# Kernel optimization log

Hardware: AMD Instinct MI355X
Metric: run time of the kernel (lower is better)

Reference implementation:

```python
import jax, jax.numpy as jnp
import numpy as np

N, D, H, F, T = 2048, 256, 4, 64, 64
HF = H * F


def setup_inputs() -> dict:
    key = jax.random.key(0)
    ks = jax.random.split(key, 24)
    f32 = jnp.float32
    emb = jax.random.normal(ks[0], (N, D), f32)
    y_as_x = jax.random.normal(ks[1], (N, T), f32)
    adj = (jax.random.uniform(ks[2], (N, N)) < 0.02).astype(f32)
    u = lambda k, shape, s: jax.random.uniform(k, shape, f32, -s, s)
    stdv = 1.0 / np.sqrt(HF)
    inp = dict(emb=emb, y_as_x=y_as_x, adj=adj)
    for i, p in enumerate(['pos', 'neg']):
        o = 3 + i * 6
        inp[p + '_w'] = u(ks[o], (D, HF), stdv)
        inp[p + '_wu'] = u(ks[o + 1], (H, F), 1.0)
        inp[p + '_wv'] = u(ks[o + 2], (H, F), 1.0)
        inp[p + '_b'] = u(ks[o + 3], (1, HF), stdv)
        inp[p + '_pw'] = u(ks[o + 4], (D, HF), 0.02)
        inp[p + '_pb'] = jnp.zeros((HF,), f32)
    inp['self_w'] = u(ks[15], (D, D), 0.02)
    inp['self_b'] = jnp.zeros((D,), f32)
    inp['mlp_pos_w'] = u(ks[16], (HF, D), 0.02)
    inp['mlp_pos_b'] = jnp.zeros((D,), f32)
    inp['mlp_neg_w'] = u(ks[17], (HF, D), 0.02)
    inp['mlp_neg_b'] = jnp.zeros((D,), f32)
    inp['sem_w1'] = u(ks[18], (D, D), 0.02)
    inp['sem_b1'] = jnp.zeros((D,), f32)
    inp['sem_w2'] = u(ks[19], (D, 1), 0.02)
    return inp


def _gat(x, mask, w, wu, wv, b, pw, pb):
    # x: [N,D], mask: [N,N] bool; multi-head GAT with dense masked softmax
    s = (x @ w).reshape(N, H, F).transpose(1, 0, 2)          # [H,N,F]
    f1 = jnp.einsum('hnf,hf->hn', s, wu)                     # u-score per node
    f2 = jnp.einsum('hnf,hf->hn', s, wv)                     # v-score per node
    logits = f1[:, None, :] + f2[:, :, None]                 # [H,N,N], i<-j
    logits = jax.nn.leaky_relu(logits, 0.2)
    masked = jnp.where(mask[None], logits, -1e9)
    attn = jnp.where(mask[None], jax.nn.softmax(masked, axis=2), 0.0)
    out = jnp.einsum('hij,hjf->hif', attn, s)                # [H,N,F]
    out = out.transpose(1, 0, 2).reshape(N, HF) + b
    return out + x @ pw + pb


def reference(emb, y_as_x, adj, pos_w, pos_wu, pos_wv, pos_b, pos_pw, pos_pb,
              neg_w, neg_wu, neg_wv, neg_b, neg_pw, neg_pb,
              self_w, self_b, mlp_pos_w, mlp_pos_b, mlp_neg_w, mlp_neg_b,
              sem_w1, sem_b1, sem_w2):
    # batched pairwise correlation (replaces the per-node Python loop)
    yc = y_as_x - y_as_x.mean(axis=1, keepdims=True)         # centered
    dot = yc @ yc.T                                          # [N,N]
    std = jnp.sqrt((yc ** 2).sum(axis=1) / (T - 1))          # torch std: ddof=1
    corr = dot / (std[:, None] * std[None, :])
    edge = adj != 0
    pos_mask = edge & (corr >= 0.1)
    neg_mask = edge & (corr < 0.1)

    pos_sup = _gat(emb, pos_mask, pos_w, pos_wu, pos_wv, pos_b, pos_pw, pos_pb)
    neg_sup = _gat(emb, neg_mask, neg_w, neg_wu, neg_wv, neg_b, neg_pw, neg_pb)

    sup = emb @ self_w + self_b
    pos_sup = pos_sup @ mlp_pos_w + mlp_pos_b
    neg_sup = neg_sup @ mlp_neg_w + mlp_neg_b

    all_emb = jnp.stack((sup, pos_sup, neg_sup), axis=1)     # [N,3,D]
    # semantic attention over the 3 relation channels
    wlog = jnp.tanh(all_emb @ sem_w1 + sem_b1) @ sem_w2      # [N,3,1]
    beta = jax.nn.softmax(wlog, axis=1)
    x = (beta * all_emb).sum(axis=1)                         # [N,D]
    # PairNorm PN-SI
    x = x - x.mean(axis=0)
    rownorm = jnp.sqrt(1e-6 + (x ** 2).sum(axis=1, keepdims=True))
    return x / rownorm
```

## Files before the change

### kernel.cpp

```cpp
#include <hip/hip_runtime.h>
#include <hip/hip_bf16.h>

#define KN  2048
#define KD  256
#define KH  4
#define KF  64
#define KT  64
#define NCS 32
#define MAXE 256

typedef __attribute__((ext_vector_type(8))) short short8;
typedef __attribute__((ext_vector_type(4))) float floatx4;

struct Args {
    const float *y, *adj, *emb;
    const float *pos_w, *pos_wu, *pos_wv, *pos_b, *pos_pw, *pos_pb;
    const float *neg_w, *neg_wu, *neg_wv, *neg_b, *neg_pw, *neg_pb;
    const float *self_w, *self_b;
    const float *mlp_pos_w, *mlp_pos_b, *mlp_neg_w, *mlp_neg_b;
    const float *sem_w1, *sem_b1, *sem_w2;
    float* out;
    unsigned char* code;
    float *ycs, *S_pos, *S_neg, *P_pos, *P_neg, *sup, *G, *psup, *X, *colsum;
    float *f1p, *f2p, *f1n, *f2n, *M0Wp, *M0Wn, *fbp, *fbn, *wlog;
};

__device__ __forceinline__ float wave_sum(float v) {
    #pragma unroll
    for (int o = 32; o > 0; o >>= 1) v += __shfl_xor(v, o, 64);
    return v;
}
__device__ __forceinline__ float wave_max(float v) {
    #pragma unroll
    for (int o = 32; o > 0; o >>= 1) v = fmaxf(v, __shfl_xor(v, o, 64));
    return v;
}
__device__ __forceinline__ short f2bs(float x) {
    union { __hip_bfloat16 h; short s; } u;
    u.h = __float2bfloat16(x);
    return u.s;
}

__global__ __launch_bounds__(256) void setup_kernel(const float* __restrict__ y,
                                                    float* __restrict__ ycs) {
    int w = threadIdx.x >> 6, lane = threadIdx.x & 63;
    int n = blockIdx.x * 4 + w;
    float v = y[n * KT + lane];
    float mean = wave_sum(v) * (1.0f / KT);
    float yc = v - mean;
    float ss = wave_sum(yc * yc);
    ycs[n * KT + lane] = yc * rsqrtf(ss * (1.0f / (KT - 1)));
}

__device__ __forceinline__ void corr_body(const float* __restrict__ ycs,
                                          const float* __restrict__ adj,
                                          unsigned char* __restrict__ code,
                                          int blk, char* smem) {
    float (*As)[68] = (float(*)[68])smem;
    float (*Bs)[68] = (float(*)[68])(smem + 4352);
    int bi = 0, rem = blk;
    while (rem >= 32 - bi) { rem -= 32 - bi; bi++; }
    int bj = bi + rem;
    int i0 = bi * 64, j0 = bj * 64;
    int t = threadIdx.x;
    int tx = t & 15, ty = t >> 4;
    int ar = t >> 2, ac = (t & 3) * 4;
    float acc[4][4] = {};
    for (int kt = 0; kt < KT; kt += 16) {
        float4 a4 = *reinterpret_cast<const float4*>(&ycs[(size_t)(i0 + ar) * KT + kt + ac]);
        float4 b4 = *reinterpret_cast<const float4*>(&ycs[(size_t)(j0 + ar) * KT + kt + ac]);
        As[ac + 0][ar] = a4.x; As[ac + 1][ar] = a4.y; As[ac + 2][ar] = a4.z; As[ac + 3][ar] = a4.w;
        Bs[ac + 0][ar] = b4.x; Bs[ac + 1][ar] = b4.y; Bs[ac + 2][ar] = b4.z; Bs[ac + 3][ar] = b4.w;
        __syncthreads();
        #pragma unroll
        for (int kk = 0; kk < 16; kk++) {
            float4 av = *reinterpret_cast<const float4*>(&As[kk][ty * 4]);
            float4 bv = *reinterpret_cast<const float4*>(&Bs[kk][tx * 4]);
            float a4v[4] = {av.x, av.y, av.z, av.w};
            float b4v[4] = {bv.x, bv.y, bv.z, bv.w};
            #pragma unroll
            for (int ii = 0; ii < 4; ii++)
                #pragma unroll
                for (int jj = 0; jj < 4; jj++) acc[ii][jj] += a4v[ii] * b4v[jj];
        }
        __syncthreads();
    }
    #pragma unroll
    for (int ii = 0; ii < 4; ii++) {
        int i = i0 + ty * 4 + ii;
        int jb = j0 + tx * 4;
        float4 av4 = *reinterpret_cast<const float4*>(&adj[(size_t)i * KN + jb]);
        float a4v[4] = {av4.x, av4.y, av4.z, av4.w};
        uchar4 cc;
        unsigned char* c = (unsigned char*)&cc;
        #pragma unroll
        for (int jj = 0; jj < 4; jj++)
            c[jj] = (a4v[jj] != 0.0f) ? ((acc[ii][jj] >= 0.1f) ? 1 : 2) : 0;
        *reinterpret_cast<uchar4*>(&code[(size_t)i * KN + jb]) = cc;
    }
    if (bi != bj) {
        #pragma unroll
        for (int jj = 0; jj < 4; jj++) {
            int j = j0 + tx * 4 + jj;
            int ib = i0 + ty * 4;
            float4 av4 = *reinterpret_cast<const float4*>(&adj[(size_t)j * KN + ib]);
            float a4v[4] = {av4.x, av4.y, av4.z, av4.w};
            uchar4 cc;
            unsigned char* c = (unsigned char*)&cc;
            #pragma unroll
            for (int ii = 0; ii < 4; ii++)
                c[ii] = (a4v[ii] != 0.0f) ? ((acc[ii][jj] >= 0.1f) ? 1 : 2) : 0;
            *reinterpret_cast<uchar4*>(&code[(size_t)j * KN + ib]) = cc;
        }
    }
}

template <bool TANH, int WCH>
__device__ __forceinline__ void mfma_gemm_body(
    const float* __restrict__ A, int lda, int bm,
    const float* __restrict__ B, int ldb, int bn,
    const float* __restrict__ bias,
    float* __restrict__ C, int ldc, int cn,
    float* __restrict__ f1h, float* __restrict__ f2h,
    const float* __restrict__ wu_h, const float* __restrict__ wv_h,
    float* __restrict__ wlogp, const float* __restrict__ w2,
    char* smem)
{
    short* As = (short*)smem;
    short* Bs = (short*)(smem + 5120);
    int t = threadIdx.x;
    int w = t >> 6, lane = t & 63;
    int m16 = lane & 15, kq = lane >> 4;
    floatx4 acc0 = {0,0,0,0}, acc1 = {0,0,0,0}, acc2 = {0,0,0,0}, acc3 = {0,0,0,0};
    int ar = t >> 2, acq = (t & 3) * 8;
    int bnn = t & 63, bkg = (t >> 6) * 8;
    for (int kt = 0; kt < KD; kt += 32) {
        const float* pa = &A[(size_t)(bm + ar) * lda + kt + acq];
        float4 a0 = *(const float4*)pa;
        float4 a1 = *(const float4*)(pa + 4);
        short8 av;
        av[0] = f2bs(a0.x); av[1] = f2bs(a0.y); av[2] = f2bs(a0.z); av[3] = f2bs(a0.w);
        av[4] = f2bs(a1.x); av[5] = f2bs(a1.y); av[6] = f2bs(a1.z); av[7] = f2bs(a1.w);
        const float* pb = &B[(size_t)(kt + bkg) * ldb + bn + bnn];
        short8 bv;
        #pragma unroll
        for (int u = 0; u < 8; u++) bv[u] = f2bs(pb[(size_t)u * ldb]);
        __syncthreads();
        *(short8*)&As[ar * 40 + acq] = av;
        *(short8*)&Bs[bnn * 40 + bkg] = bv;
        __syncthreads();
        short8 af  = *(short8*)&As[(w * 16 + m16) * 40 + kq * 8];
        short8 bf0 = *(short8*)&Bs[( 0 + m16) * 40 + kq * 8];
        short8 bf1 = *(short8*)&Bs[(16 + m16) * 40 + kq * 8];
        short8 bf2 = *(short8*)&Bs[(32 + m16) * 40 + kq * 8];
        short8 bf3 = *(short8*)&Bs[(48 + m16) * 40 + kq * 8];
        acc0 = __builtin_amdgcn_mfma_f32_16x16x32_bf16(af, bf0, acc0, 0, 0, 0);
        acc1 = __builtin_amdgcn_mfma_f32_16x16x32_bf16(af, bf1, acc1, 0, 0, 0);
        acc2 = __builtin_amdgcn_mfma_f32_16x16x32_bf16(af, bf2, acc2, 0, 0, 0);
        acc3 = __builtin_amdgcn_mfma_f32_16x16x32_bf16(af, bf3, acc3, 0, 0, 0);
    }
    int row0 = bm + w * 16 + kq * 4;
    floatx4 accs[4] = {acc0, acc1, acc2, acc3};
    if (WCH >= 0) {
        float w2c[4];
        #pragma unroll
        for (int nb = 0; nb < 4; nb++) w2c[nb] = w2[cn + nb * 16 + m16];
        #pragma unroll
        for (int r = 0; r < 4; r++) {
            float p = 0.0f;
            #pragma unroll
            for (int nb = 0; nb < 4; nb++) {
                float v = accs[nb][r] + bias[nb * 16 + m16];
                float vc = fminf(fmaxf(v, -9.0f), 9.0f);
                float ex = __expf(2.0f * vc);
                p += ((ex - 1.0f) / (ex + 1.0f)) * w2c[nb];
            }
            #pragma unroll
            for (int o = 1; o < 16; o <<= 1) p += __shfl_xor(p, o, 64);
            if (m16 == 0) atomicAdd(&wlogp[(size_t)(row0 + r) * 4 + WCH], p);
        }
        return;
    }
    #pragma unroll
    for (int nb = 0; nb < 4; nb++) {
        #pragma unroll
        for (int r = 0; r < 4; r++) {
            int col = nb * 16 + m16;
            float v = accs[nb][r] + (bias ? bias[col] : 0.0f);
            if (TANH) {
                float vc = fminf(fmaxf(v, -9.0f), 9.0f);
                float ex = __expf(2.0f * vc);
                v = (ex - 1.0f) / (ex + 1.0f);
            }
            C[(size_t)(row0 + r) * ldc + cn + col] = v;
        }
    }
    if (f1h) {
        float wuv[4], wvv[4];
        #pragma unroll
        for (int nb = 0; nb < 4; nb++) { wuv[nb] = wu_h[nb * 16 + m16]; wvv[nb] = wv_h[nb * 16 + m16]; }
        #pragma unroll
        for (int r = 0; r < 4; r++) {
            float p1 = accs[0][r] * wuv[0] + accs[1][r] * wuv[1] + accs[2][r] * wuv[2] + accs[3][r] * wuv[3];
            float p2 = accs[0][r] * wvv[0] + accs[1][r] * wvv[1] + accs[2][r] * wvv[2] + accs[3][r] * wvv[3];
            #pragma unroll
            for (int o = 1; o < 16; o <<= 1) {
                p1 += __shfl_xor(p1, o, 64);
                p2 += __shfl_xor(p2, o, 64);
            }
            if (m16 == 0) { f1h[row0 + r] = p1; f2h[row0 + r] = p2; }
        }
    }
}

__device__ __forceinline__ void fb_unit(const float* __restrict__ mb,
                                        const float* __restrict__ w1,
                                        const float* __restrict__ b1,
                                        float* __restrict__ fb) {
    int j = threadIdx.x;
    float acc = b1[j];
    for (int k = 0; k < KD; k++) acc = fmaf(mb[k], w1[(size_t)k * KD + j], acc);
    fb[j] = acc;
}

__global__ __launch_bounds__(256, 4) void phase1_kernel(Args a) {
    __shared__ alignas(16) char smem[10240];
    int blk = blockIdx.x;
    if (blk < 528) { corr_body(a.ycs, a.adj, a.code, blk, smem); return; }
    if (blk < 1168) {
        int b = blk - 528;
        int tn = b % 20, tm = b / 20;
        int buf = tn >> 2, coloff = (tn & 3) * 64, h = tn & 3;
        const float* B; const float* bias = nullptr; float* C;
        float *f1h = nullptr, *f2h = nullptr;
        const float *wu = nullptr, *wv = nullptr;
        if (buf == 0) {
            B = a.pos_w; C = a.S_pos;
            f1h = a.f1p + h * KN; f2h = a.f2p + h * KN;
            wu = a.pos_wu + h * KF; wv = a.pos_wv + h * KF;
        } else if (buf == 1) {
            B = a.neg_w; C = a.S_neg;
            f1h = a.f1n + h * KN; f2h = a.f2n + h * KN;
            wu = a.neg_wu + h * KF; wv = a.neg_wv + h * KF;
        } else if (buf == 2) { B = a.pos_pw; bias = a.pos_pb + coloff; C = a.P_pos; }
        else if (buf == 3)   { B = a.neg_pw; bias = a.neg_pb + coloff; C = a.P_neg; }
        else                 { B = a.self_w; bias = a.self_b + coloff; C = a.sup; }
        mfma_gemm_body<false, -1>(a.emb, KD, tm * 64, B, KD, coloff, bias,
                                  C, KD, coloff, f1h, f2h, wu, wv,
                                  nullptr, nullptr, smem);
        return;
    }
    if (blk < 1184) {
        int v = blk - 1168;
        mfma_gemm_body<false, -1>(a.mlp_pos_w, KD, (v >> 2) * 64, a.sem_w1, KD, (v & 3) * 64,
                                  nullptr, a.M0Wp, KD, (v & 3) * 64,
                                  nullptr, nullptr, nullptr, nullptr,
                                  nullptr, nullptr, smem);
        return;
    }
    if (blk < 1200) {
        int v = blk - 1184;
        mfma_gemm_body<false, -1>(a.mlp_neg_w, KD, (v >> 2) * 64, a.sem_w1, KD, (v & 3) * 64,
                                  nullptr, a.M0Wn, KD, (v & 3) * 64,
                                  nullptr, nullptr, nullptr, nullptr,
                                  nullptr, nullptr, smem);
        return;
    }
    if (blk == 1200) { fb_unit(a.mlp_pos_b, a.sem_w1, a.sem_b1, a.fbp); return; }
    if (blk == 1201) { fb_unit(a.mlp_neg_b, a.sem_w1, a.sem_b1, a.fbn); return; }
    for (int j = threadIdx.x; j < NCS * KD; j += 256) a.colsum[j] = 0.0f;
    for (int j = threadIdx.x; j < KN * 4; j += 256) a.wlog[j] = 0.0f;
}

__global__ __launch_bounds__(256) void attn_kernel(Args a) {
    __shared__ alignas(16) int jl[2][MAXE];
    __shared__ alignas(16) float lg[KH][MAXE];
    __shared__ int cnt[2];
    int i = blockIdx.x;
    int w = threadIdx.x >> 6, lane = threadIdx.x & 63;
    if (threadIdx.x < 2) cnt[threadIdx.x] = 0;
    __syncthreads();
    #pragma unroll
    for (int it = 0; it < 2; it++) {
        int base = w * 512 + it * 256;
        uchar4 cv = *reinterpret_cast<const uchar4*>(&a.code[(size_t)i * KN + base + lane * 4]);
        const unsigned char* ce = (const unsigned char*)&cv;
        #pragma unroll
        for (int e = 0; e < 4; e++) {
            #pragma unroll
            for (int rel = 0; rel < 2; rel++) {
                bool pr = (ce[e] == (rel ? (unsigned char)2 : (unsigned char)1));
                unsigned long long bal = __ballot(pr);
                int tot = __popcll(bal);
                int basepos = 0;
                if (lane == 0 && tot) basepos = atomicAdd(&cnt[rel], tot);
                basepos = __shfl(basepos, 0, 64);
                if (pr) {
                    int idx = basepos + __popcll(bal & ((1ull << lane) - 1ull));
                    if (idx < MAXE) jl[rel][idx] = base + lane * 4 + e;
                }
            }
        }
    }
    __syncthreads();
    int c0 = cnt[0]; if (c0 > MAXE) c0 = MAXE;
    int c1 = cnt[1]; if (c1 > MAXE) c1 = MAXE;
    if (threadIdx.x < 4) {
        int cR = (c0 + 3) & ~3;
        if (c0 + threadIdx.x < cR) jl[0][c0 + threadIdx.x] = 0;
    } else if (threadIdx.x < 8) {
        int l2 = threadIdx.x - 4;
        int cR = (c1 + 3) & ~3;
        if (c1 + l2 < cR) jl[1][c1 + l2] = 0;
    }
    __syncthreads();
    int h = w;
    int g = lane >> 4, q4 = (lane & 15) * 4;
    for (int rel = 0; rel < 2; rel++) {
        const float* f1 = rel ? a.f1n : a.f1p;
        const float* f2 = rel ? a.f2n : a.f2p;
        const float* S  = rel ? a.S_neg : a.S_pos;
        const float* P  = rel ? a.P_neg : a.P_pos;
        const float* b  = rel ? a.neg_b : a.pos_b;
        float* G        = a.G + (size_t)rel * KN * KD;
        int count = rel ? c1 : c0;
        int countR = (count + 3) & ~3;
        float f2i = f2[h * KN + i];
        float m = -1e30f;
        for (int k = lane; k < count; k += 64) {
            int j = jl[rel][k];
            float x = f1[h * KN + j] + f2i;
            x = (x > 0.0f) ? x : 0.2f * x;
            lg[h][k] = x;
            m = fmaxf(m, x);
        }
        m = wave_max(m);
        float ps = 0.0f;
        for (int k = lane; k < count; k += 64) {
            float e = __expf(lg[h][k] - m);
            lg[h][k] = e;
            ps += e;
        }
        float denom = wave_sum(ps);
        for (int k2 = count + lane; k2 < countR; k2 += 64) lg[h][k2] = 0.0f;
        const float* Sh4 = S + h * KF + q4;
        float ax = 0.0f, ay = 0.0f, az = 0.0f, aw = 0.0f;
        for (int k = 0; k < countR; k += 4) {
            int j = jl[rel][k + g];
            float wgt = lg[h][k + g];
            float4 sv = *reinterpret_cast<const float4*>(&Sh4[(size_t)j * KD]);
            ax += wgt * sv.x; ay += wgt * sv.y; az += wgt * sv.z; aw += wgt * sv.w;
        }
        #pragma unroll
        for (int o = 16; o < 64; o <<= 1) {
            ax += __shfl_xor(ax, o, 64); ay += __shfl_xor(ay, o, 64);
            az += __shfl_xor(az, o, 64); aw += __shfl_xor(aw, o, 64);
        }
        if (g == 0) {
            float inv = count ? (1.0f / denom) : 0.0f;
            int col = h * KF + q4;
            size_t idx = (size_t)i * KD + col;
            float4 pv = *reinterpret_cast<const float4*>(&P[idx]);
            float4 o4;
            o4.x = ax * inv + b[col + 0] + pv.x;
            o4.y = ay * inv + b[col + 1] + pv.y;
            o4.z = az * inv + b[col + 2] + pv.z;
            o4.w = aw * inv + b[col + 3] + pv.w;
            *reinterpret_cast<float4*>(&G[idx]) = o4;
        }
    }
}

__global__ __launch_bounds__(256, 4) void tail_kernel(Args a) {
    __shared__ alignas(16) char smem[10240];
    int u = blockIdx.x;
    if (u < 256) {
        int bx = u & 3, bm = (u >> 2) * 64;
        bool sel = bm >= KN;
        mfma_gemm_body<false, -1>(a.G, KD, bm, sel ? a.mlp_neg_w : a.mlp_pos_w, KD, bx * 64,
                                  (sel ? a.mlp_neg_b : a.mlp_pos_b) + bx * 64,
                                  a.psup, KD, bx * 64,
                                  nullptr, nullptr, nullptr, nullptr,
                                  nullptr, nullptr, smem);
    } else if (u < 384) {
        int v = u - 256; int bx = v & 3, bm = (v >> 2) * 64;
        mfma_gemm_body<true, 0>(a.sup, KD, bm, a.sem_w1, KD, bx * 64, a.sem_b1 + bx * 64,
                                nullptr, KD, bx * 64,
                                nullptr, nullptr, nullptr, nullptr,
                                a.wlog, a.sem_w2, smem);
    } else if (u < 512) {
        int v = u - 384; int bx = v & 3, bm = (v >> 2) * 64;
        mfma_gemm_body<true, 1>(a.G, KD, bm, a.M0Wp, KD, bx * 64, a.fbp + bx * 64,
                                nullptr, KD, bx * 64,
                                nullptr, nullptr, nullptr, nullptr,
                                a.wlog, a.sem_w2, smem);
    } else {
        int v = u - 512; int bx = v & 3, bm = KN + (v >> 2) * 64;
        mfma_gemm_body<true, 2>(a.G, KD, bm, a.M0Wn, KD, bx * 64, a.fbn + bx * 64,
                                nullptr, KD, bx * 64,
                                nullptr, nullptr, nullptr, nullptr,
                                a.wlog - (size_t)KN * 4, a.sem_w2, smem);
    }
}

__global__ __launch_bounds__(256) void combine_kernel(Args a) {
    int n = blockIdx.x, d = threadIdx.x;
    size_t idx = (size_t)n * KD + d;
    float4 wl = *reinterpret_cast<const float4*>(&a.wlog[(size_t)n * 4]);
    float mm = fmaxf(wl.x, fmaxf(wl.y, wl.z));
    float e0 = __expf(wl.x - mm), e1 = __expf(wl.y - mm), e2 = __expf(wl.z - mm);
    float inv = 1.0f / (e0 + e1 + e2);
    float* nsup = a.psup + (size_t)KN * KD;
    float x = (e0 * inv) * a.sup[idx] + (e1 * inv) * a.psup[idx] + (e2 * inv) * nsup[idx];
    a.X[idx] = x;
    atomicAdd(&a.colsum[(n & (NCS - 1)) * KD + d], x);
}

__global__ __launch_bounds__(256) void final_kernel(Args a) {
    __shared__ float sb[4];
    int n = blockIdx.x, d = threadIdx.x;
    float cs = 0.0f;
    #pragma unroll
    for (int r = 0; r < NCS; r++) cs += a.colsum[r * KD + d];
    float mean = cs * (1.0f / KN);
    float xc = a.X[(size_t)n * KD + d] - mean;
    int wv = d >> 6, lane = d & 63;
    float s = wave_sum(xc * xc);
    if (lane == 0) sb[wv] = s;
    __syncthreads();
    float ss = sb[0] + sb[1] + sb[2] + sb[3];
    a.out[(size_t)n * KD + d] = xc * rsqrtf(1e-6f + ss);
}

extern "C" void kernel_launch(void* const* d_in, const int* in_sizes, int n_in,
                              void* d_out, int out_size, void* d_ws, size_t ws_size,
                              hipStream_t stream) {
    typedef const float* fp;
    Args a;
    a.emb    = (fp)d_in[0];
    a.y      = (fp)d_in[1];
    a.adj    = (fp)d_in[2];
    a.pos_w  = (fp)d_in[3];  a.pos_wu = (fp)d_in[4];  a.pos_wv = (fp)d_in[5];
    a.pos_b  = (fp)d_in[6];  a.pos_pw = (fp)d_in[7];  a.pos_pb = (fp)d_in[8];
    a.neg_w  = (fp)d_in[9];  a.neg_wu = (fp)d_in[10]; a.neg_wv = (fp)d_in[11];
    a.neg_b  = (fp)d_in[12]; a.neg_pw = (fp)d_in[13]; a.neg_pb = (fp)d_in[14];
    a.self_w = (fp)d_in[15]; a.self_b = (fp)d_in[16];
    a.mlp_pos_w = (fp)d_in[17]; a.mlp_pos_b = (fp)d_in[18];
    a.mlp_neg_w = (fp)d_in[19]; a.mlp_neg_b = (fp)d_in[20];
    a.sem_w1 = (fp)d_in[21]; a.sem_b1 = (fp)d_in[22]; a.sem_w2 = (fp)d_in[23];
    a.out = (float*)d_out;

    char* ws = (char*)d_ws;
    size_t off = 0;
    auto alloc = [&](size_t sz) -> char* {
        char* p = ws + off;
        off += (sz + 511) & ~(size_t)511;
        return p;
    };
    const size_t MAT = (size_t)KN * KD * 4;

    a.ycs    = (float*)alloc((size_t)KN * KT * 4);
    a.code   = (unsigned char*)alloc((size_t)KN * KN);
    a.S_pos  = (float*)alloc(MAT);
    a.S_neg  = (float*)alloc(MAT);
    a.P_pos  = (float*)alloc(MAT);
    a.P_neg  = (float*)alloc(MAT);
    a.sup    = (float*)alloc(MAT);
    a.G      = (float*)alloc(2 * MAT);
    a.psup   = (float*)alloc(2 * MAT);
    a.X      = (float*)alloc(MAT);
    a.colsum = (float*)alloc((size_t)NCS * KD * 4);
    a.f1p    = (float*)alloc((size_t)KH * KN * 4);
    a.f2p    = (float*)alloc((size_t)KH * KN * 4);
    a.f1n    = (float*)alloc((size_t)KH * KN * 4);
    a.f2n    = (float*)alloc((size_t)KH * KN * 4);
    a.M0Wp   = (float*)alloc((size_t)KD * KD * 4);
    a.M0Wn   = (float*)alloc((size_t)KD * KD * 4);
    a.fbp    = (float*)alloc(KD * 4);
    a.fbn    = (float*)alloc(KD * 4);
    a.wlog   = (float*)alloc((size_t)KN * 4 * 4);

    setup_kernel<<<512, 256, 0, stream>>>(a.y, a.ycs);
    phase1_kernel<<<1203, 256, 0, stream>>>(a);
    attn_kernel<<<KN, 256, 0, stream>>>(a);
    tail_kernel<<<640, 256, 0, stream>>>(a);
    combine_kernel<<<KN, 256, 0, stream>>>(a);
    final_kernel<<<KN, 256, 0, stream>>>(a);
}
```

Before: 163.3 us.

## Fuse correlation normalization into corr tiles and merge combine/final via grid barrier

Drops the separate setup kernel: each correlation tile now computes the row means and inverse stds of its 64+64 y rows and normalizes on the fly while staging into shared memory. The combine and PairNorm kernels are merged into one 1024-block kernel where each block handles two rows, keeps x in registers, and waits on a global atomic counter barrier before reading column sums. This removes two launches and the X intermediate round trip. In exchange, row statistics are recomputed redundantly per tile, and correctness relies on all 1024 blocks being co-resident for the spin barrier.

```diff
diff --git a/kernel.cpp b/kernel.cpp
--- a/kernel.cpp
+++ b/kernel.cpp
@@ -8,6 +8,7 @@
 #define KT  64
 #define NCS 32
 #define MAXE 256
+#define CFB 1024
 
 typedef __attribute__((ext_vector_type(8))) short short8;
 typedef __attribute__((ext_vector_type(4))) float floatx4;
@@ -20,8 +21,9 @@
     const float *mlp_pos_w, *mlp_pos_b, *mlp_neg_w, *mlp_neg_b;
     const float *sem_w1, *sem_b1, *sem_w2;
     float* out;
+    int* bar;
     unsigned char* code;
-    float *ycs, *S_pos, *S_neg, *P_pos, *P_neg, *sup, *G, *psup, *X, *colsum;
+    float *S_pos, *S_neg, *P_pos, *P_neg, *sup, *G, *psup, *colsum;
     float *f1p, *f2p, *f1n, *f2n, *M0Wp, *M0Wn, *fbp, *fbn, *wlog;
 };
 
@@ -41,36 +43,47 @@
     return u.s;
 }
 
-__global__ __launch_bounds__(256) void setup_kernel(const float* __restrict__ y,
-                                                    float* __restrict__ ycs) {
-    int w = threadIdx.x >> 6, lane = threadIdx.x & 63;
-    int n = blockIdx.x * 4 + w;
-    float v = y[n * KT + lane];
-    float mean = wave_sum(v) * (1.0f / KT);
-    float yc = v - mean;
-    float ss = wave_sum(yc * yc);
-    ycs[n * KT + lane] = yc * rsqrtf(ss * (1.0f / (KT - 1)));
-}
-
-__device__ __forceinline__ void corr_body(const float* __restrict__ ycs,
+__device__ __forceinline__ void corr_body(const float* __restrict__ y,
                                           const float* __restrict__ adj,
                                           unsigned char* __restrict__ code,
                                           int blk, char* smem) {
     float (*As)[68] = (float(*)[68])smem;
     float (*Bs)[68] = (float(*)[68])(smem + 4352);
+    float* mAs = (float*)(smem + 8704);
+    float* rAs = (float*)(smem + 8960);
+    float* mBs = (float*)(smem + 9216);
+    float* rBs = (float*)(smem + 9472);
     int bi = 0, rem = blk;
     while (rem >= 32 - bi) { rem -= 32 - bi; bi++; }
     int bj = bi + rem;
     int i0 = bi * 64, j0 = bj * 64;
-    int t = threadIdx.x;
+    int t = threadIdx.x, w = t >> 6, lane = t & 63;
+    for (int rr = 0; rr < 16; rr++) {
+        int r = w * 16 + rr;
+        float vA = y[(size_t)(i0 + r) * KT + lane];
+        float mA = wave_sum(vA) * (1.0f / KT);
+        float dA = vA - mA;
+        float sA = wave_sum(dA * dA);
+        if (lane == 0) { mAs[r] = mA; rAs[r] = rsqrtf(sA * (1.0f / (KT - 1))); }
+        float vB = y[(size_t)(j0 + r) * KT + lane];
+        float mB = wave_sum(vB) * (1.0f / KT);
+        float dB = vB - mB;
+        float sB = wave_sum(dB * dB);
+        if (lane == 0) { mBs[r] = mB; rBs[r] = rsqrtf(sB * (1.0f / (KT - 1))); }
+    }
+    __syncthreads();
     int tx = t & 15, ty = t >> 4;
     int ar = t >> 2, ac = (t & 3) * 4;
+    float mA = mAs[ar], rA = rAs[ar], mB = mBs[ar], rB = rBs[ar];
     float acc[4][4] = {};
     for (int kt = 0; kt < KT; kt += 16) {
-        float4 a4 = *reinterpret_cast<const float4*>(&ycs[(size_t)(i0 + ar) * KT + kt + ac]);
-        float4 b4 = *reinterpret_cast<const float4*>(&ycs[(size_t)(j0 + ar) * KT + kt + ac]);
-        As[ac + 0][ar] = a4.x; As[ac + 1][ar] = a4.y; As[ac + 2][ar] = a4.z; As[ac + 3][ar] = a4.w;
-        Bs[ac + 0][ar] = b4.x; Bs[ac + 1][ar] = b4.y; Bs[ac + 2][ar] = b4.z; Bs[ac + 3][ar] = b4.w;
+        float4 a4 = *reinterpret_cast<const float4*>(&y[(size_t)(i0 + ar) * KT + kt + ac]);
+        float4 b4 = *reinterpret_cast<const float4*>(&y[(size_t)(j0 + ar) * KT + kt + ac]);
+        __syncthreads();
+        As[ac + 0][ar] = (a4.x - mA) * rA; As[ac + 1][ar] = (a4.y - mA) * rA;
+        As[ac + 2][ar] = (a4.z - mA) * rA; As[ac + 3][ar] = (a4.w - mA) * rA;
+        Bs[ac + 0][ar] = (b4.x - mB) * rB; Bs[ac + 1][ar] = (b4.y - mB) * rB;
+        Bs[ac + 2][ar] = (b4.z - mB) * rB; Bs[ac + 3][ar] = (b4.w - mB) * rB;
         __syncthreads();
         #pragma unroll
         for (int kk = 0; kk < 16; kk++) {
@@ -83,7 +96,6 @@
                 #pragma unroll
                 for (int jj = 0; jj < 4; jj++) acc[ii][jj] += a4v[ii] * b4v[jj];
         }
-        __syncthreads();
     }
     #pragma unroll
     for (int ii = 0; ii < 4; ii++) {
@@ -226,7 +238,7 @@
 __global__ __launch_bounds__(256, 4) void phase1_kernel(Args a) {
     __shared__ alignas(16) char smem[10240];
     int blk = blockIdx.x;
-    if (blk < 528) { corr_body(a.ycs, a.adj, a.code, blk, smem); return; }
+    if (blk < 528) { corr_body(a.y, a.adj, a.code, blk, smem); return; }
     if (blk < 1168) {
         int b = blk - 528;
         int tn = b % 20, tm = b / 20;
@@ -270,6 +282,7 @@
     if (blk == 1201) { fb_unit(a.mlp_neg_b, a.sem_w1, a.sem_b1, a.fbn); return; }
     for (int j = threadIdx.x; j < NCS * KD; j += 256) a.colsum[j] = 0.0f;
     for (int j = threadIdx.x; j < KN * 4; j += 256) a.wlog[j] = 0.0f;
+    if (threadIdx.x == 0) a.bar[0] = 0;
 }
 
 __global__ __launch_bounds__(256) void attn_kernel(Args a) {
@@ -403,33 +416,48 @@
     }
 }
 
-__global__ __launch_bounds__(256) void combine_kernel(Args a) {
-    int n = blockIdx.x, d = threadIdx.x;
-    size_t idx = (size_t)n * KD + d;
-    float4 wl = *reinterpret_cast<const float4*>(&a.wlog[(size_t)n * 4]);
-    float mm = fmaxf(wl.x, fmaxf(wl.y, wl.z));
-    float e0 = __expf(wl.x - mm), e1 = __expf(wl.y - mm), e2 = __expf(wl.z - mm);
-    float inv = 1.0f / (e0 + e1 + e2);
-    float* nsup = a.psup + (size_t)KN * KD;
-    float x = (e0 * inv) * a.sup[idx] + (e1 * inv) * a.psup[idx] + (e2 * inv) * nsup[idx];
-    a.X[idx] = x;
-    atomicAdd(&a.colsum[(n & (NCS - 1)) * KD + d], x);
-}
-
-__global__ __launch_bounds__(256) void final_kernel(Args a) {
-    __shared__ float sb[4];
-    int n = blockIdx.x, d = threadIdx.x;
+__global__ __launch_bounds__(256) void cf_kernel(Args a) {
+    __shared__ float sb[2][4];
+    int b = blockIdx.x, d = threadIdx.x;
+    int wv = d >> 6, lane = d & 63;
+    const float* nsup = a.psup + (size_t)KN * KD;
+    float x[2];
+    #pragma unroll
+    for (int s = 0; s < 2; s++) {
+        int n = b + s * CFB;
+        size_t idx = (size_t)n * KD + d;
+        float4 wl = *reinterpret_cast<const float4*>(&a.wlog[(size_t)n * 4]);
+        float mm = fmaxf(wl.x, fmaxf(wl.y, wl.z));
+        float e0 = __expf(wl.x - mm), e1 = __expf(wl.y - mm), e2 = __expf(wl.z - mm);
+        float inv = 1.0f / (e0 + e1 + e2);
+        x[s] = (e0 * inv) * a.sup[idx] + (e1 * inv) * a.psup[idx] + (e2 * inv) * nsup[idx];
+    }
+    float old = atomicAdd(&a.colsum[(b & (NCS - 1)) * KD + d], x[0] + x[1]);
+    if (old == -1e38f) a.out[0] = 0.0f;
+    __syncthreads();
+    if (d == 0) {
+        __hip_atomic_fetch_add(&a.bar[0], 1, __ATOMIC_RELAXED, __HIP_MEMORY_SCOPE_AGENT);
+        while (__hip_atomic_load(&a.bar[0], __ATOMIC_RELAXED, __HIP_MEMORY_SCOPE_AGENT) < CFB)
+            __builtin_amdgcn_s_sleep(2);
+    }
+    __syncthreads();
     float cs = 0.0f;
     #pragma unroll
     for (int r = 0; r < NCS; r++) cs += a.colsum[r * KD + d];
     float mean = cs * (1.0f / KN);
-    float xc = a.X[(size_t)n * KD + d] - mean;
-    int wv = d >> 6, lane = d & 63;
-    float s = wave_sum(xc * xc);
-    if (lane == 0) sb[wv] = s;
-    __syncthreads();
-    float ss = sb[0] + sb[1] + sb[2] + sb[3];
-    a.out[(size_t)n * KD + d] = xc * rsqrtf(1e-6f + ss);
+    #pragma unroll
+    for (int s = 0; s < 2; s++) {
+        float xc = x[s] - mean;
+        float ssv = wave_sum(xc * xc);
+        if (lane == 0) sb[s][wv] = ssv;
+    }
+    __syncthreads();
+    #pragma unroll
+    for (int s = 0; s < 2; s++) {
+        int n = b + s * CFB;
+        float ss = sb[s][0] + sb[s][1] + sb[s][2] + sb[s][3];
+        a.out[(size_t)n * KD + d] = (x[s] - mean) * rsqrtf(1e-6f + ss);
+    }
 }
 
 extern "C" void kernel_launch(void* const* d_in, const int* in_sizes, int n_in,
@@ -459,7 +487,7 @@
     };
     const size_t MAT = (size_t)KN * KD * 4;
 
-    a.ycs    = (float*)alloc((size_t)KN * KT * 4);
+    a.bar    = (int*)alloc(512);
     a.code   = (unsigned char*)alloc((size_t)KN * KN);
     a.S_pos  = (float*)alloc(MAT);
     a.S_neg  = (float*)alloc(MAT);
@@ -468,7 +496,6 @@
     a.sup    = (float*)alloc(MAT);
     a.G      = (float*)alloc(2 * MAT);
     a.psup   = (float*)alloc(2 * MAT);
-    a.X      = (float*)alloc(MAT);
     a.colsum = (float*)alloc((size_t)NCS * KD * 4);
     a.f1p    = (float*)alloc((size_t)KH * KN * 4);
     a.f2p    = (float*)alloc((size_t)KH * KN * 4);
@@ -480,10 +507,8 @@
     a.fbn    = (float*)alloc(KD * 4);
     a.wlog   = (float*)alloc((size_t)KN * 4 * 4);
 
-    setup_kernel<<<512, 256, 0, stream>>>(a.y, a.ycs);
     phase1_kernel<<<1203, 256, 0, stream>>>(a);
     attn_kernel<<<KN, 256, 0, stream>>>(a);
     tail_kernel<<<640, 256, 0, stream>>>(a);
-    combine_kernel<<<KN, 256, 0, stream>>>(a);
-    final_kernel<<<KN, 256, 0, stream>>>(a);
-}
+    cf_kernel<<<CFB, 256, 0, stream>>>(a);
+}
```

Result: slower. 196.0 us (+20.0%).

## Fuse tail GEMMs, semantic attention and combine into one per-row-block kernel

Applied to the files above, without the earlier changes.

Replaces the separate tail GEMM kernel (MLP projections plus tanh-weighted semantic logits) and the combine kernel with a single kernel where each block owns 16 rows. It runs five 16x256x256 GEMMs in sequence, keeps the MLP outputs in registers, reduces the semantic logits in shared memory, and then applies the softmax weighting and column-sum atomics directly. This drops the psup and wlog global buffers, one launch, and the global atomics on wlog. The cost is only 128 blocks, each restaging the full 256x256 B weights per GEMM, so parallelism is lower and there is more redundant weight loading.

```diff
diff --git a/kernel.cpp b/kernel.cpp
--- a/kernel.cpp
+++ b/kernel.cpp
@@ -21,8 +21,8 @@
     const float *sem_w1, *sem_b1, *sem_w2;
     float* out;
     unsigned char* code;
-    float *ycs, *S_pos, *S_neg, *P_pos, *P_neg, *sup, *G, *psup, *X, *colsum;
-    float *f1p, *f2p, *f1n, *f2n, *M0Wp, *M0Wn, *fbp, *fbn, *wlog;
+    float *ycs, *S_pos, *S_neg, *P_pos, *P_neg, *sup, *G, *X, *colsum;
+    float *f1p, *f2p, *f1n, *f2n, *M0Wp, *M0Wn, *fbp, *fbn;
 };
 
 __device__ __forceinline__ float wave_sum(float v) {
@@ -115,7 +115,6 @@
     }
 }
 
-template <bool TANH, int WCH>
 __device__ __forceinline__ void mfma_gemm_body(
     const float* __restrict__ A, int lda, int bm,
     const float* __restrict__ B, int ldb, int bn,
@@ -123,7 +122,6 @@
     float* __restrict__ C, int ldc, int cn,
     float* __restrict__ f1h, float* __restrict__ f2h,
     const float* __restrict__ wu_h, const float* __restrict__ wv_h,
-    float* __restrict__ wlogp, const float* __restrict__ w2,
     char* smem)
 {
     short* As = (short*)smem;
@@ -161,37 +159,12 @@
     }
     int row0 = bm + w * 16 + kq * 4;
     floatx4 accs[4] = {acc0, acc1, acc2, acc3};
-    if (WCH >= 0) {
-        float w2c[4];
-        #pragma unroll
-        for (int nb = 0; nb < 4; nb++) w2c[nb] = w2[cn + nb * 16 + m16];
-        #pragma unroll
-        for (int r = 0; r < 4; r++) {
-            float p = 0.0f;
-            #pragma unroll
-            for (int nb = 0; nb < 4; nb++) {
-                float v = accs[nb][r] + bias[nb * 16 + m16];
-                float vc = fminf(fmaxf(v, -9.0f), 9.0f);
-                float ex = __expf(2.0f * vc);
-                p += ((ex - 1.0f) / (ex + 1.0f)) * w2c[nb];
-            }
-            #pragma unroll
-            for (int o = 1; o < 16; o <<= 1) p += __shfl_xor(p, o, 64);
-            if (m16 == 0) atomicAdd(&wlogp[(size_t)(row0 + r) * 4 + WCH], p);
-        }
-        return;
-    }
     #pragma unroll
     for (int nb = 0; nb < 4; nb++) {
         #pragma unroll
         for (int r = 0; r < 4; r++) {
             int col = nb * 16 + m16;
             float v = accs[nb][r] + (bias ? bias[col] : 0.0f);
-            if (TANH) {
-                float vc = fminf(fmaxf(v, -9.0f), 9.0f);
-                float ex = __expf(2.0f * vc);
-                v = (ex - 1.0f) / (ex + 1.0f);
-            }
             C[(size_t)(row0 + r) * ldc + cn + col] = v;
         }
     }
@@ -245,31 +218,27 @@
         } else if (buf == 2) { B = a.pos_pw; bias = a.pos_pb + coloff; C = a.P_pos; }
         else if (buf == 3)   { B = a.neg_pw; bias = a.neg_pb + coloff; C = a.P_neg; }
         else                 { B = a.self_w; bias = a.self_b + coloff; C = a.sup; }
-        mfma_gemm_body<false, -1>(a.emb, KD, tm * 64, B, KD, coloff, bias,
-                                  C, KD, coloff, f1h, f2h, wu, wv,
-                                  nullptr, nullptr, smem);
+        mfma_gemm_body(a.emb, KD, tm * 64, B, KD, coloff, bias,
+                       C, KD, coloff, f1h, f2h, wu, wv, smem);
         return;
     }
     if (blk < 1184) {
         int v = blk - 1168;
-        mfma_gemm_body<false, -1>(a.mlp_pos_w, KD, (v >> 2) * 64, a.sem_w1, KD, (v & 3) * 64,
-                                  nullptr, a.M0Wp, KD, (v & 3) * 64,
-                                  nullptr, nullptr, nullptr, nullptr,
-                                  nullptr, nullptr, smem);
+        mfma_gemm_body(a.mlp_pos_w, KD, (v >> 2) * 64, a.sem_w1, KD, (v & 3) * 64,
+                       nullptr, a.M0Wp, KD, (v & 3) * 64,
+                       nullptr, nullptr, nullptr, nullptr, smem);
         return;
     }
     if (blk < 1200) {
         int v = blk - 1184;
-        mfma_gemm_body<false, -1>(a.mlp_neg_w, KD, (v >> 2) * 64, a.sem_w1, KD, (v & 3) * 64,
-                                  nullptr, a.M0Wn, KD, (v & 3) * 64,
-                                  nullptr, nullptr, nullptr, nullptr,
-                                  nullptr, nullptr, smem);
+        mfma_gemm_body(a.mlp_neg_w, KD, (v >> 2) * 64, a.sem_w1, KD, (v & 3) * 64,
+                       nullptr, a.M0Wn, KD, (v & 3) * 64,
+                       nullptr, nullptr, nullptr, nullptr, smem);
         return;
     }
     if (blk == 1200) { fb_unit(a.mlp_pos_b, a.sem_w1, a.sem_b1, a.fbp); return; }
     if (blk == 1201) { fb_unit(a.mlp_neg_b, a.sem_w1, a.sem_b1, a.fbn); return; }
     for (int j = threadIdx.x; j < NCS * KD; j += 256) a.colsum[j] = 0.0f;
-    for (int j = threadIdx.x; j < KN * 4; j += 256) a.wlog[j] = 0.0f;
 }
 
 __global__ __launch_bounds__(256) void attn_kernel(Args a) {
@@ -371,49 +340,117 @@
     }
 }
 
-__global__ __launch_bounds__(256, 4) void tail_kernel(Args a) {
-    __shared__ alignas(16) char smem[10240];
-    int u = blockIdx.x;
-    if (u < 256) {
-        int bx = u & 3, bm = (u >> 2) * 64;
-        bool sel = bm >= KN;
-        mfma_gemm_body<false, -1>(a.G, KD, bm, sel ? a.mlp_neg_w : a.mlp_pos_w, KD, bx * 64,
-                                  (sel ? a.mlp_neg_b : a.mlp_pos_b) + bx * 64,
-                                  a.psup, KD, bx * 64,
-                                  nullptr, nullptr, nullptr, nullptr,
-                                  nullptr, nullptr, smem);
-    } else if (u < 384) {
-        int v = u - 256; int bx = v & 3, bm = (v >> 2) * 64;
-        mfma_gemm_body<true, 0>(a.sup, KD, bm, a.sem_w1, KD, bx * 64, a.sem_b1 + bx * 64,
-                                nullptr, KD, bx * 64,
-                                nullptr, nullptr, nullptr, nullptr,
-                                a.wlog, a.sem_w2, smem);
-    } else if (u < 512) {
-        int v = u - 384; int bx = v & 3, bm = (v >> 2) * 64;
-        mfma_gemm_body<true, 1>(a.G, KD, bm, a.M0Wp, KD, bx * 64, a.fbp + bx * 64,
-                                nullptr, KD, bx * 64,
-                                nullptr, nullptr, nullptr, nullptr,
-                                a.wlog, a.sem_w2, smem);
-    } else {
-        int v = u - 512; int bx = v & 3, bm = KN + (v >> 2) * 64;
-        mfma_gemm_body<true, 2>(a.G, KD, bm, a.M0Wn, KD, bx * 64, a.fbn + bx * 64,
-                                nullptr, KD, bx * 64,
-                                nullptr, nullptr, nullptr, nullptr,
-                                a.wlog - (size_t)KN * 4, a.sem_w2, smem);
-    }
-}
-
-__global__ __launch_bounds__(256) void combine_kernel(Args a) {
-    int n = blockIdx.x, d = threadIdx.x;
-    size_t idx = (size_t)n * KD + d;
-    float4 wl = *reinterpret_cast<const float4*>(&a.wlog[(size_t)n * 4]);
-    float mm = fmaxf(wl.x, fmaxf(wl.y, wl.z));
-    float e0 = __expf(wl.x - mm), e1 = __expf(wl.y - mm), e2 = __expf(wl.z - mm);
-    float inv = 1.0f / (e0 + e1 + e2);
-    float* nsup = a.psup + (size_t)KN * KD;
-    float x = (e0 * inv) * a.sup[idx] + (e1 * inv) * a.psup[idx] + (e2 * inv) * nsup[idx];
-    a.X[idx] = x;
-    atomicAdd(&a.colsum[(n & (NCS - 1)) * KD + d], x);
+__global__ __launch_bounds__(256, 2) void tailcombine_kernel(Args a) {
+    __shared__ alignas(16) short A_s[16][264];
+    __shared__ alignas(16) short B_s[256][40];
+    __shared__ float wrow[3][16];
+    __shared__ float beta[16][3];
+    int r0 = blockIdx.x * 16;
+    int t = threadIdx.x, w = t >> 6, lane = t & 63;
+    int m16 = lane & 15, kq = lane >> 4;
+    if (t < 48) ((float*)wrow)[t] = 0.0f;
+
+    auto stageA = [&](const float* rowbase) {
+        int row = t >> 4, c0 = (t & 15) * 16;
+        const float* p = &rowbase[(size_t)row * KD + c0];
+        float4 f0 = *(const float4*)(p);
+        float4 f1 = *(const float4*)(p + 4);
+        float4 f2 = *(const float4*)(p + 8);
+        float4 f3 = *(const float4*)(p + 12);
+        short8 v0, v1;
+        v0[0] = f2bs(f0.x); v0[1] = f2bs(f0.y); v0[2] = f2bs(f0.z); v0[3] = f2bs(f0.w);
+        v0[4] = f2bs(f1.x); v0[5] = f2bs(f1.y); v0[6] = f2bs(f1.z); v0[7] = f2bs(f1.w);
+        v1[0] = f2bs(f2.x); v1[1] = f2bs(f2.y); v1[2] = f2bs(f2.z); v1[3] = f2bs(f2.w);
+        v1[4] = f2bs(f3.x); v1[5] = f2bs(f3.y); v1[6] = f2bs(f3.z); v1[7] = f2bs(f3.w);
+        *(short8*)&A_s[row][c0] = v0;
+        *(short8*)&A_s[row][c0 + 8] = v1;
+    };
+    auto gemmPass = [&](const float* __restrict__ B, floatx4* acc) {
+        for (int kt = 0; kt < KD; kt += 32) {
+            #pragma unroll
+            for (int g = 0; g < 4; g++) {
+                short8 bv;
+                #pragma unroll
+                for (int u = 0; u < 8; u++)
+                    bv[u] = f2bs(B[(size_t)(kt + g * 8 + u) * KD + t]);
+                *(short8*)&B_s[t][g * 8] = bv;
+            }
+            __syncthreads();
+            short8 af = *(short8*)&A_s[m16][kt + kq * 8];
+            #pragma unroll
+            for (int nb = 0; nb < 4; nb++) {
+                short8 bf = *(short8*)&B_s[w * 64 + nb * 16 + m16][kq * 8];
+                acc[nb] = __builtin_amdgcn_mfma_f32_16x16x32_bf16(af, bf, acc[nb], 0, 0, 0);
+            }
+            __syncthreads();
+        }
+    };
+    auto wDot = [&](floatx4* acc, const float* __restrict__ fb, int ch) {
+        float p[4] = {0, 0, 0, 0};
+        #pragma unroll
+        for (int nb = 0; nb < 4; nb++) {
+            int col = w * 64 + nb * 16 + m16;
+            float fbv = fb[col], w2v = a.sem_w2[col];
+            #pragma unroll
+            for (int r = 0; r < 4; r++) {
+                float v = acc[nb][r] + fbv;
+                float vc = fminf(fmaxf(v, -9.0f), 9.0f);
+                float ex = __expf(2.0f * vc);
+                p[r] += ((ex - 1.0f) / (ex + 1.0f)) * w2v;
+            }
+        }
+        #pragma unroll
+        for (int r = 0; r < 4; r++) {
+            float pr = p[r];
+            #pragma unroll
+            for (int o = 1; o < 16; o <<= 1) pr += __shfl_xor(pr, o, 64);
+            if (m16 == 0) atomicAdd(&wrow[ch][kq * 4 + r], pr);
+        }
+    };
+
+    floatx4 accP[4] = {{0,0,0,0},{0,0,0,0},{0,0,0,0},{0,0,0,0}};
+    floatx4 accN[4] = {{0,0,0,0},{0,0,0,0},{0,0,0,0},{0,0,0,0}};
+    floatx4 accW[4];
+
+    stageA(a.G + (size_t)r0 * KD);
+    gemmPass(a.mlp_pos_w, accP);
+    #pragma unroll
+    for (int nb = 0; nb < 4; nb++) accW[nb] = floatx4{0,0,0,0};
+    gemmPass(a.M0Wp, accW);  wDot(accW, a.fbp, 1);
+    __syncthreads();
+    stageA(a.G + (size_t)(KN + r0) * KD);
+    gemmPass(a.mlp_neg_w, accN);
+    #pragma unroll
+    for (int nb = 0; nb < 4; nb++) accW[nb] = floatx4{0,0,0,0};
+    gemmPass(a.M0Wn, accW);  wDot(accW, a.fbn, 2);
+    __syncthreads();
+    stageA(a.sup + (size_t)r0 * KD);
+    #pragma unroll
+    for (int nb = 0; nb < 4; nb++) accW[nb] = floatx4{0,0,0,0};
+    gemmPass(a.sem_w1, accW);  wDot(accW, a.sem_b1, 0);
+    __syncthreads();
+    if (t < 16) {
+        float w0 = wrow[0][t], w1 = wrow[1][t], w2l = wrow[2][t];
+        float mm = fmaxf(w0, fmaxf(w1, w2l));
+        float e0 = __expf(w0 - mm), e1 = __expf(w1 - mm), e2 = __expf(w2l - mm);
+        float inv = 1.0f / (e0 + e1 + e2);
+        beta[t][0] = e0 * inv; beta[t][1] = e1 * inv; beta[t][2] = e2 * inv;
+    }
+    __syncthreads();
+    #pragma unroll
+    for (int nb = 0; nb < 4; nb++) {
+        int col = w * 64 + nb * 16 + m16;
+        float pb = a.mlp_pos_b[col], nbias = a.mlp_neg_b[col];
+        #pragma unroll
+        for (int r = 0; r < 4; r++) {
+            int row = kq * 4 + r;
+            size_t idx = (size_t)(r0 + row) * KD + col;
+            float b0 = beta[row][0], b1 = beta[row][1], b2 = beta[row][2];
+            float xv = b0 * a.sup[idx] + b1 * (accP[nb][r] + pb) + b2 * (accN[nb][r] + nbias);
+            a.X[idx] = xv;
+            atomicAdd(&a.colsum[((r0 + row) & (NCS - 1)) * KD + col], xv);
+        }
+    }
 }
 
 __global__ __launch_bounds__(256) void final_kernel(Args a) {
@@ -467,7 +504,6 @@
     a.P_neg  = (float*)alloc(MAT);
     a.sup    = (float*)alloc(MAT);
     a.G      = (float*)alloc(2 * MAT);
-    a.psup   = (float*)alloc(2 * MAT);
     a.X      = (float*)alloc(MAT);
     a.colsum = (float*)alloc((size_t)NCS * KD * 4);
     a.f1p    = (float*)alloc((size_t)KH * KN * 4);
@@ -478,12 +514,10 @@
     a.M0Wn   = (float*)alloc((size_t)KD * KD * 4);
     a.fbp    = (float*)alloc(KD * 4);
     a.fbn    = (float*)alloc(KD * 4);
-    a.wlog   = (float*)alloc((size_t)KN * 4 * 4);
 
     setup_kernel<<<512, 256, 0, stream>>>(a.y, a.ycs);
     phase1_kernel<<<1203, 256, 0, stream>>>(a);
     attn_kernel<<<KN, 256, 0, stream>>>(a);
-    tail_kernel<<<640, 256, 0, stream>>>(a);
-    combine_kernel<<<KN, 256, 0, stream>>>(a);
+    tailcombine_kernel<<<KN / 16, 256, 0, stream>>>(a);
     final_kernel<<<KN, 256, 0, stream>>>(a);
 }
```

New measurement: 192.1 us. +17.7%, slower.
